# Performance work log

Measured on AMD Instinct MI355X. Metric: run time of the kernel, lower is better.

Reference implementation:

```python
import jax, jax.numpy as jnp
import numpy as np
import math

DIM = 1536
NH = 12
HD = 128          # head_dim
C = HD // 2       # 64 complex rope dims
MAX_ATTN = 15 * 880
EPS = 1e-6


def _rope_tables(max_len=1024, d=HD, theta=10000.0):
    # Wan rope_params: freqs = cat([rope(1024, d-4*(d//6)), rope(1024, 2*(d//6)), rope(1024, 2*(d//6))], dim=1)
    d0 = d - 4 * (d // 6)   # 44 -> 22 complex dims (F axis)
    d1 = 2 * (d // 6)       # 42 -> 21 complex dims (H and W axes)
    parts = []
    for dd in (d0, d1, d1):
        inv = 1.0 / theta ** (np.arange(0, dd, 2, dtype=np.float32) / dd)
        parts.append(np.outer(np.arange(max_len, dtype=np.float32), inv))
    ang = np.concatenate(parts, axis=1)                 # [1024, C]
    return np.stack([np.cos(ang), np.sin(ang)], -1)     # [1024, C, 2]


def rmsnorm(x, g, eps=EPS):
    return x * jax.lax.rsqrt(jnp.mean(x * x, axis=-1, keepdims=True) + eps) * g


def rope_apply(xq, f, h, w, freqs, start_frame):
    # xq: [B, S, N, D]; freqs: [1024, C, 2] cos/sin tables; S = f*h*w
    b, s, n, d = xq.shape
    c = d // 2
    s0 = c - 2 * (c // 3)   # F-axis complex dims (22)
    s1 = c // 3             # H/W-axis complex dims (21)
    cos, sin = freqs[..., 0], freqs[..., 1]

    def per_token(tab):
        tf = jnp.broadcast_to(tab[start_frame:start_frame + f, :s0][:, None, None, :], (f, h, w, s0))
        th = jnp.broadcast_to(tab[:h, s0:s0 + s1][None, :, None, :], (f, h, w, s1))
        tw = jnp.broadcast_to(tab[:w, s0 + s1:][None, None, :, :], (f, h, w, s1))
        return jnp.concatenate([tf, th, tw], -1).reshape(1, s, 1, c)

    pc, ps = per_token(cos), per_token(sin)
    xr = xq.reshape(b, s, n, c, 2)
    re, im = xr[..., 0], xr[..., 1]
    out = jnp.stack([re * pc - im * ps, re * ps + im * pc], -1)
    return out.reshape(b, s, n, d)


def _forward(x, wq, bq, wk, bk, wv, bv, wo, bo, gq, gk, freqs, k_cache, v_cache, f, h, w, current_start):
    b, s, _ = x.shape
    frame_seqlen = h * w
    start_frame = current_start // frame_seqlen

    q = rmsnorm(x @ wq.T + bq, gq).reshape(b, s, NH, HD)
    k = rmsnorm(x @ wk.T + bk, gk).reshape(b, s, NH, HD)
    v = (x @ wv.T + bv).reshape(b, s, NH, HD)

    rq = rope_apply(q, f, h, w, freqs, start_frame)
    rk = rope_apply(k, f, h, w, freqs, start_frame)

    current_end = current_start + s
    # cache not full: append new keys/values at [current_start:current_end]
    k_cache = jax.lax.dynamic_update_slice(k_cache, rk, (0, current_start, 0, 0))
    v_cache = jax.lax.dynamic_update_slice(v_cache, v, (0, current_start, 0, 0))

    win_start = max(0, current_end - MAX_ATTN)
    kk = k_cache[:, win_start:current_end]   # [B, Lk, N, D]
    vv = v_cache[:, win_start:current_end]

    scale = 1.0 / math.sqrt(HD)
    scores = jnp.einsum('bqnd,bknd->bnqk', rq, kk) * scale
    attn = jax.nn.softmax(scores, axis=-1)
    out = jnp.einsum('bnqk,bknd->bqnd', attn, vv).reshape(b, s, DIM)
    return out @ wo.T + bo


def setup_inputs() -> dict:
    key = jax.random.key(0)
    ks = jax.random.split(key, 8)
    B, S, CACHE = 1, 880, 18 * 880
    x = jax.random.normal(ks[0], (B, S, DIM), jnp.float32)

    def lin(k):
        k1, k2 = jax.random.split(k)
        wgt = jax.random.normal(k1, (DIM, DIM), jnp.float32) / math.sqrt(DIM)
        bia = jax.random.normal(k2, (DIM,), jnp.float32) * 0.01
        return wgt, bia

    wq, bq = lin(ks[1]); wk, bk = lin(ks[2]); wv, bv = lin(ks[3]); wo, bo = lin(ks[4])
    gq = jnp.ones((DIM,), jnp.float32)
    gk = jnp.ones((DIM,), jnp.float32)
    freqs = jnp.asarray(_rope_tables())
    k_cache = jax.random.normal(ks[5], (B, CACHE, NH, HD), jnp.float32) * 0.5
    v_cache = jax.random.normal(ks[6], (B, CACHE, NH, HD), jnp.float32) * 0.5
    grid_sizes = jnp.array([1, 22, 40], jnp.int32)  # (F, H, W), H*W = 880
    return dict(x=x, wq=wq, bq=bq, wk=wk, bk=bk, wv=wv, bv=bv, wo=wo, bo=bo,
                gq=gq, gk=gk, freqs=freqs, k_cache=k_cache, v_cache=v_cache,
                grid_sizes=grid_sizes, current_start=10560)


def reference(x, wq, bq, wk, bk, wv, bv, wo, bo, gq, gk, freqs, k_cache, v_cache, grid_sizes, current_start):
    f, h, w = (int(grid_sizes[0]), int(grid_sizes[1]), int(grid_sizes[2]))
    return _forward(x, wq, bq, wk, bk, wv, bv, wo, bo, gq, gk, freqs,
                    k_cache, v_cache, f, h, w, int(current_start))
```

## Files before the change

### kernel.cpp

```cpp
#include <hip/hip_runtime.h>

#define NHEADS 12
#define HDIM 128
#define MODEL_DIM 1536
#define MAX_ATTN_W 13200
#define NSPLIT 12

typedef unsigned short u16;
typedef unsigned int u32;
typedef float f32x4 __attribute__((ext_vector_type(4)));
typedef float f32x16 __attribute__((ext_vector_type(16)));
typedef __bf16 bf16x8 __attribute__((ext_vector_type(8)));

static __device__ __forceinline__ u16 f2bf(float f) {
  union { __bf16 h; u16 u; } cv;
  cv.h = (__bf16)f;
  return cv.u;
}
static __device__ __forceinline__ float bf2f(u16 u) {
  union { u32 u; float f; } cv;
  cv.u = ((u32)u) << 16;
  return cv.f;
}

__global__ void k_conv_bf16(const float* __restrict__ src, u16* __restrict__ dst, int n4) {
  int i = blockIdx.x * blockDim.x + threadIdx.x;
  if (i >= n4) return;
  float4 v = ((const float4*)src)[i];
  u32 lo = (u32)f2bf(v.x) | ((u32)f2bf(v.y) << 16);
  u32 hi = (u32)f2bf(v.z) | ((u32)f2bf(v.w) << 16);
  ((uint2*)dst)[i] = make_uint2(lo, hi);
}

__global__ void k_conv_bf16_w4(const float* __restrict__ s0, const float* __restrict__ s1,
                               const float* __restrict__ s2, const float* __restrict__ s3,
                               u16* __restrict__ d0, u16* __restrict__ d1,
                               u16* __restrict__ d2, u16* __restrict__ d3, int n4) {
  int i = blockIdx.x * blockDim.x + threadIdx.x;
  if (i >= n4) return;
  const int which = blockIdx.y;
  const float* src = (which == 0) ? s0 : (which == 1) ? s1 : (which == 2) ? s2 : s3;
  u16* dst = (which == 0) ? d0 : (which == 1) ? d1 : (which == 2) ? d2 : d3;
  float4 v = ((const float4*)src)[i];
  u32 lo = (u32)f2bf(v.x) | ((u32)f2bf(v.y) << 16);
  u32 hi = (u32)f2bf(v.z) | ((u32)f2bf(v.w) << 16);
  ((uint2*)dst)[i] = make_uint2(lo, hi);
}

__global__ void k_build_kold(const float* __restrict__ kc, u16* __restrict__ K_all,
                             const int* __restrict__ csp, int S, int KVcap) {
  const int cs = csp[0];
  const int ce = cs + S;
  int wst = ce - MAX_ATTN_W; if (wst < 0) wst = 0;
  const int oldlen = cs - wst;
  const long per = (long)oldlen * 16;
  const long total = per * NHEADS;
  for (long c = blockIdx.x * (long)blockDim.x + threadIdx.x; c < total;
       c += (long)gridDim.x * blockDim.x) {
    int n = (int)(c / per);
    long r = c - (long)n * per;
    int jo = (int)(r >> 4);
    int dc = ((int)r & 15) * 8;
    const float* s = kc + ((size_t)(wst + jo) * NHEADS + n) * HDIM + dc;
    float4 a = *(const float4*)s;
    float4 b = *(const float4*)(s + 4);
    uint4 o;
    o.x = (u32)f2bf(a.x) | ((u32)f2bf(a.y) << 16);
    o.y = (u32)f2bf(a.z) | ((u32)f2bf(a.w) << 16);
    o.z = (u32)f2bf(b.x) | ((u32)f2bf(b.y) << 16);
    o.w = (u32)f2bf(b.z) | ((u32)f2bf(b.w) << 16);
    *(uint4*)(K_all + ((size_t)n * KVcap + jo) * HDIM + dc) = o;
  }
}

__launch_bounds__(256)
__global__ void k_build_vtold(const float* __restrict__ vc, u16* __restrict__ VT,
                              const int* __restrict__ csp, int S, int KVcap) {
  __shared__ u16 tile[64][130];
  const int cs = csp[0];
  const int ce = cs + S;
  int wst = ce - MAX_ATTN_W; if (wst < 0) wst = 0;
  const int oldlen = cs - wst;
  const int n = blockIdx.y;
  const int j0 = blockIdx.x * 64;
  if (j0 >= oldlen) return;
  const int tid = threadIdx.x;

  #pragma unroll
  for (int i = 0; i < 8; i++) {
    int idx = tid + 256 * i;
    int j = idx >> 5;
    int dc = (idx & 31) * 4;
    float4 v = make_float4(0.f, 0.f, 0.f, 0.f);
    if (j0 + j < oldlen)
      v = *(const float4*)(vc + ((size_t)(wst + j0 + j) * NHEADS + n) * HDIM + dc);
    u32 lo = (u32)f2bf(v.x) | ((u32)f2bf(v.y) << 16);
    u32 hi = (u32)f2bf(v.z) | ((u32)f2bf(v.w) << 16);
    *(u32*)&tile[j][dc] = lo;
    *(u32*)&tile[j][dc + 2] = hi;
  }
  __syncthreads();

  const int d = tid >> 1;
  const int jh = (tid & 1) * 32;
  alignas(16) u16 buf[32];
  #pragma unroll
  for (int j = 0; j < 32; j++) buf[j] = tile[jh + j][d];
  u16* dst = VT + ((size_t)n * HDIM + d) * KVcap + j0 + jh;
  if (j0 + jh + 32 <= oldlen) {
    #pragma unroll
    for (int c = 0; c < 4; c++)
      *(uint4*)(dst + c * 8) = *(const uint4*)&buf[c * 8];
  } else {
    for (int j = 0; j < 32 && j0 + jh + j < oldlen; j++) dst[j] = buf[j];
  }
}

__launch_bounds__(256)
__global__ void k_gemm_o128(const u16* __restrict__ A, const u16* __restrict__ B,
                            const float* __restrict__ bias, float* __restrict__ out,
                            int M, int N, int K) {
  __shared__ __align__(16) u16 Al[128][40];
  __shared__ __align__(16) u16 Bl[128][40];
  const int n0 = blockIdx.y * 128;
  const int tid = threadIdx.x;
  const int wid = tid >> 6, l = tid & 63, l31 = l & 31, hi = l >> 5;
  const int wr = wid >> 1, wc = wid & 1;
  const int m0 = blockIdx.x * 128;
  f32x16 acc[2][2];
  #pragma unroll
  for (int mt = 0; mt < 2; mt++)
    #pragma unroll
    for (int nt = 0; nt < 2; nt++)
      #pragma unroll
      for (int j = 0; j < 16; j++) acc[mt][nt][j] = 0.f;
  const int row = tid >> 2, colc = (tid & 3) * 8;
  for (int k0 = 0; k0 < K; k0 += 32) {
    __syncthreads();
    uint4 a0 = *(const uint4*)(A + (size_t)(m0 + row) * K + k0 + colc);
    uint4 a1 = *(const uint4*)(A + (size_t)(m0 + row + 64) * K + k0 + colc);
    uint4 b0 = *(const uint4*)(B + (size_t)(n0 + row) * K + k0 + colc);
    uint4 b1 = *(const uint4*)(B + (size_t)(n0 + row + 64) * K + k0 + colc);
    *(uint4*)&Al[row][colc] = a0;
    *(uint4*)&Al[row + 64][colc] = a1;
    *(uint4*)&Bl[row][colc] = b0;
    *(uint4*)&Bl[row + 64][colc] = b1;
    __syncthreads();
    #pragma unroll
    for (int ks = 0; ks < 2; ks++) {
      bf16x8 af[2], bfr[2];
      #pragma unroll
      for (int mt = 0; mt < 2; mt++)
        af[mt] = *(const bf16x8*)&Al[wr * 64 + mt * 32 + l31][ks * 16 + hi * 8];
      #pragma unroll
      for (int nt = 0; nt < 2; nt++)
        bfr[nt] = *(const bf16x8*)&Bl[wc * 64 + nt * 32 + l31][ks * 16 + hi * 8];
      #pragma unroll
      for (int mt = 0; mt < 2; mt++)
        #pragma unroll
        for (int nt = 0; nt < 2; nt++)
          acc[mt][nt] = __builtin_amdgcn_mfma_f32_32x32x16_bf16(af[mt], bfr[nt], acc[mt][nt], 0, 0, 0);
    }
  }
  #pragma unroll
  for (int mt = 0; mt < 2; mt++)
    #pragma unroll
    for (int nt = 0; nt < 2; nt++) {
      const int col = n0 + wc * 64 + nt * 32 + l31;
      const float bb = bias[col];
      #pragma unroll
      for (int r = 0; r < 16; r++) {
        int rowo = m0 + wr * 64 + mt * 32 + (r & 3) + 8 * (r >> 2) + 4 * hi;
        if (rowo < M) out[(size_t)rowo * N + col] = acc[mt][nt][r] + bb;
      }
    }
}

__launch_bounds__(256)
__global__ void k_gemm_qkv128(const u16* __restrict__ A,
                              const u16* __restrict__ B0, const u16* __restrict__ B1,
                              const u16* __restrict__ B2,
                              const float* __restrict__ bias0, const float* __restrict__ bias1,
                              const float* __restrict__ bias2,
                              float* __restrict__ o0, float* __restrict__ o1, float* __restrict__ o2,
                              int M, int N, int K) {
  __shared__ __align__(16) u16 Al[128][40];
  __shared__ __align__(16) u16 Bl[128][40];
  const int nblk = N / 128;
  const int which = blockIdx.y / nblk;
  const int n0 = (blockIdx.y % nblk) * 128;
  const u16* B = (which == 0) ? B0 : ((which == 1) ? B1 : B2);
  const float* bias = (which == 0) ? bias0 : ((which == 1) ? bias1 : bias2);
  float* out = (which == 0) ? o0 : ((which == 1) ? o1 : o2);
  const int tid = threadIdx.x;
  const int wid = tid >> 6, l = tid & 63, l31 = l & 31, hi = l >> 5;
  const int wr = wid >> 1, wc = wid & 1;
  const int m0 = blockIdx.x * 128;
  f32x16 acc[2][2];
  #pragma unroll
  for (int mt = 0; mt < 2; mt++)
    #pragma unroll
    for (int nt = 0; nt < 2; nt++)
      #pragma unroll
      for (int j = 0; j < 16; j++) acc[mt][nt][j] = 0.f;
  const int row = tid >> 2, colc = (tid & 3) * 8;
  for (int k0 = 0; k0 < K; k0 += 32) {
    __syncthreads();
    uint4 a0 = *(const uint4*)(A + (size_t)(m0 + row) * K + k0 + colc);
    uint4 a1 = *(const uint4*)(A + (size_t)(m0 + row + 64) * K + k0 + colc);
    uint4 b0 = *(const uint4*)(B + (size_t)(n0 + row) * K + k0 + colc);
    uint4 b1 = *(const uint4*)(B + (size_t)(n0 + row + 64) * K + k0 + colc);
    *(uint4*)&Al[row][colc] = a0;
    *(uint4*)&Al[row + 64][colc] = a1;
    *(uint4*)&Bl[row][colc] = b0;
    *(uint4*)&Bl[row + 64][colc] = b1;
    __syncthreads();
    #pragma unroll
    for (int ks = 0; ks < 2; ks++) {
      bf16x8 af[2], bfr[2];
      #pragma unroll
      for (int mt = 0; mt < 2; mt++)
        af[mt] = *(const bf16x8*)&Al[wr * 64 + mt * 32 + l31][ks * 16 + hi * 8];
      #pragma unroll
      for (int nt = 0; nt < 2; nt++)
        bfr[nt] = *(const bf16x8*)&Bl[wc * 64 + nt * 32 + l31][ks * 16 + hi * 8];
      #pragma unroll
      for (int mt = 0; mt < 2; mt++)
        #pragma unroll
        for (int nt = 0; nt < 2; nt++)
          acc[mt][nt] = __builtin_amdgcn_mfma_f32_32x32x16_bf16(af[mt], bfr[nt], acc[mt][nt], 0, 0, 0);
    }
  }
  #pragma unroll
  for (int mt = 0; mt < 2; mt++)
    #pragma unroll
    for (int nt = 0; nt < 2; nt++) {
      const int col = n0 + wc * 64 + nt * 32 + l31;
      const float bb = bias[col];
      #pragma unroll
      for (int r = 0; r < 16; r++) {
        int rowo = m0 + wr * 64 + mt * 32 + (r & 3) + 8 * (r >> 2) + 4 * hi;
        if (rowo < M) out[(size_t)rowo * N + col] = acc[mt][nt][r] + bb;
      }
    }
}

__launch_bounds__(256)
__global__ void k_norm_rope(const float* __restrict__ qp, const float* __restrict__ kp,
                            const float* __restrict__ vp, const float* __restrict__ gq,
                            const float* __restrict__ gk, const float* __restrict__ freqs,
                            const int* __restrict__ gs, const int* __restrict__ csp,
                            int S, int KVcap,
                            u16* __restrict__ rq, u16* __restrict__ K_all,
                            u16* __restrict__ VT) {
  const int t = blockIdx.x;
  const int tid = threadIdx.x;
  const float* q = qp + (size_t)t * MODEL_DIM;
  const float* k = kp + (size_t)t * MODEL_DIM;
  const float* v = vp + (size_t)t * MODEL_DIM;
  float sq = 0.f, sk = 0.f;
  for (int j = tid; j < MODEL_DIM; j += 256) {
    float a = q[j]; sq += a * a;
    float b = k[j]; sk += b * b;
  }
  #pragma unroll
  for (int off = 32; off > 0; off >>= 1) {
    sq += __shfl_down(sq, off, 64);
    sk += __shfl_down(sk, off, 64);
  }
  __shared__ float red[8];
  int wv_ = tid >> 6, l = tid & 63;
  if (l == 0) { red[wv_] = sq; red[4 + wv_] = sk; }
  __syncthreads();
  sq = red[0] + red[1] + red[2] + red[3];
  sk = red[4] + red[5] + red[6] + red[7];
  const float rq_s = rsqrtf(sq * (1.0f / MODEL_DIM) + 1e-6f) * 0.12751744f;
  const float rk_s = rsqrtf(sk * (1.0f / MODEL_DIM) + 1e-6f);

  const int cs = csp[0];
  const int h = gs[1], ww = gs[2];
  const int hw = h * ww;
  const int sf = cs / hw;
  const int fi = t / hw;
  const int rr = t - fi * hw;
  const int hi = rr / ww;
  const int wi = rr - hi * ww;
  const int ce = cs + S;
  int wst = ce - MAX_ATTN_W; if (wst < 0) wst = 0;
  const int jj = cs + t - wst;

  for (int p = tid; p < NHEADS * 64; p += 256) {
    int n = p >> 6, c = p & 63;
    int pos = (c < 22) ? (sf + fi) : ((c < 43) ? hi : wi);
    float cv = freqs[(pos * 64 + c) * 2];
    float sv = freqs[(pos * 64 + c) * 2 + 1];
    int j0 = n * HDIM + 2 * c;
    float qr = q[j0] * rq_s * gq[j0];
    float qi = q[j0 + 1] * rq_s * gq[j0 + 1];
    u32 oq = (u32)f2bf(qr * cv - qi * sv) | ((u32)f2bf(qr * sv + qi * cv) << 16);
    *(u32*)(rq + ((size_t)n * S + t) * HDIM + 2 * c) = oq;
    float kr = k[j0] * rk_s * gk[j0];
    float ki = k[j0 + 1] * rk_s * gk[j0 + 1];
    u32 ok = (u32)f2bf(kr * cv - ki * sv) | ((u32)f2bf(kr * sv + ki * cv) << 16);
    *(u32*)(K_all + ((size_t)n * KVcap + jj) * HDIM + 2 * c) = ok;
  }
  for (int j = tid; j < MODEL_DIM; j += 256) {
    int n = j >> 7, d = j & 127;
    VT[((size_t)n * HDIM + d) * KVcap + jj] = f2bf(v[j]);
  }
}

__launch_bounds__(256, 2)
__global__ void k_attn_split(const u16* __restrict__ rq, const u16* __restrict__ K_all,
                             const u16* __restrict__ VT,
                             u16* __restrict__ po, float* __restrict__ pm, float* __restrict__ pl,
                             const int* __restrict__ csp, int S, int KVcap) {
  __shared__ __align__(16) u16 Klds[2][64][128];
  __shared__ __align__(16) u16 Vlds[2][128][64];

  const int tid = threadIdx.x;
  const int wid = tid >> 6;
  const int l = tid & 63;
  const int l31 = l & 31;
  const int hi = l >> 5;
  const int swz = (l31 & 7) << 3;
  const int head = blockIdx.y;
  const int split = blockIdx.z;
  const int q0 = blockIdx.x * 128;

  const int cs = csp[0];
  const int ce = cs + S;
  int wst = ce - MAX_ATTN_W; if (wst < 0) wst = 0;
  const int KV = ce - wst;
  const int chunk = (((KV + NSPLIT - 1) / NSPLIT) + 63) & ~63;
  const int kstart = split * chunk;
  int kend = kstart + chunk; if (kend > KV) kend = KV;

  const size_t pbase = ((size_t)head * NSPLIT + split) * S;
  const int qrow = q0 + wid * 32 + l31;

  if (kstart >= kend) {
    if (qrow < S && hi == 0) { pm[pbase + qrow] = -3.0e38f; pl[pbase + qrow] = 0.f; }
    return;
  }

  bf16x8 qf[8];
  if (qrow < S) {
    const u16* qp = rq + ((size_t)head * S + qrow) * HDIM;
    #pragma unroll
    for (int ds = 0; ds < 8; ds++) qf[ds] = *(const bf16x8*)(qp + ds * 16 + hi * 8);
  } else {
    #pragma unroll
    for (int ds = 0; ds < 8; ds++)
      #pragma unroll
      for (int i = 0; i < 8; i++) qf[ds][i] = (__bf16)0.0f;
  }

  f32x16 o[4];
  #pragma unroll
  for (int dt = 0; dt < 4; dt++)
    #pragma unroll
    for (int j = 0; j < 16; j++) o[dt][j] = 0.f;
  float m_ = -3.0e38f, lsum_ = 0.f;

  const u16* Kh = K_all + (size_t)head * KVcap * HDIM;
  const u16* Vh = VT + (size_t)head * HDIM * KVcap;

  uint4 kr[4], vr[4];
  auto load_tile = [&](int key0) {
    #pragma unroll
    for (int i = 0; i < 4; i++) {
      int cid = tid + 256 * i;
      int krow = cid >> 4;
      int gk_ = key0 + krow;
      kr[i] = make_uint4(0, 0, 0, 0);
      if (gk_ < kend) kr[i] = *(const uint4*)(Kh + (size_t)gk_ * HDIM + (cid & 15) * 8);
    }
    #pragma unroll
    for (int i = 0; i < 4; i++) {
      int cid = tid + 256 * i;
      int d = cid >> 3;
      int kc = (cid & 7) * 8;
      const u16* src = Vh + (size_t)d * KVcap + key0 + kc;
      if (key0 + kc + 8 <= kend) {
        vr[i] = *(const uint4*)src;
      } else {
        alignas(16) u16 tmp[8];
        #pragma unroll
        for (int j = 0; j < 8; j++) tmp[j] = (key0 + kc + j < kend) ? src[j] : (u16)0;
        vr[i] = *(const uint4*)tmp;
      }
    }
  };
  auto stage_to = [&](int p) {
    #pragma unroll
    for (int i = 0; i < 4; i++) {
      int cid = tid + 256 * i;
      int krow = cid >> 4;
      *(uint4*)&Klds[p][krow][((cid & 15) * 8) ^ ((krow & 7) << 3)] = kr[i];
    }
    #pragma unroll
    for (int i = 0; i < 4; i++) {
      int cid = tid + 256 * i;
      int d = cid >> 3;
      *(uint4*)&Vlds[p][d][((cid & 7) * 8) ^ ((d & 7) << 3)] = vr[i];
    }
  };

  const int ntiles = (kend - kstart + 63) >> 6;
  load_tile(kstart);
  stage_to(0);
  if (ntiles > 1) load_tile(kstart + 64);

  for (int t = 0; t < ntiles; t++) {
    const int key0 = kstart + (t << 6);
    const int cur = t & 1;
    __syncthreads();
    if (t + 1 < ntiles) stage_to(cur ^ 1);
    if (t + 2 < ntiles) load_tile(key0 + 128);

    f32x16 s[2];
    __builtin_amdgcn_s_setprio(1);
    #pragma unroll
    for (int kt = 0; kt < 2; kt++) {
      #pragma unroll
      for (int j = 0; j < 16; j++) s[kt][j] = 0.f;
      #pragma unroll
      for (int ds = 0; ds < 8; ds++) {
        bf16x8 kf = *(const bf16x8*)&Klds[cur][kt * 32 + l31][(ds * 16 + hi * 8) ^ swz];
        s[kt] = __builtin_amdgcn_mfma_f32_32x32x16_bf16(kf, qf[ds], s[kt], 0, 0, 0);
      }
    }
    __builtin_amdgcn_s_setprio(0);

    float tm = -3.0e38f;
    if (key0 + 64 <= kend) {
      #pragma unroll
      for (int kt = 0; kt < 2; kt++)
        #pragma unroll
        for (int r = 0; r < 16; r++) tm = fmaxf(tm, s[kt][r]);
    } else {
      #pragma unroll
      for (int kt = 0; kt < 2; kt++) {
        const int rem = kend - key0 - kt * 32;
        #pragma unroll
        for (int r = 0; r < 16; r++) {
          const int off = (r & 3) + 8 * (r >> 2) + 4 * hi;
          float v = (off < rem) ? s[kt][r] : -3.0e38f;
          s[kt][r] = v;
          tm = fmaxf(tm, v);
        }
      }
    }
    tm = fmaxf(tm, __shfl_xor(tm, 32, 64));

    if (!__all(tm <= m_ + 8.0f)) {
      float nm = fmaxf(m_, tm);
      float alpha = exp2f(m_ - nm);
      m_ = nm;
      lsum_ *= alpha;
      #pragma unroll
      for (int dt = 0; dt < 4; dt++)
        #pragma unroll
        for (int j = 0; j < 16; j++) o[dt][j] *= alpha;
    }

    float rs = 0.f;
    u32 w[2][8];
    #pragma unroll
    for (int kt = 0; kt < 2; kt++)
      #pragma unroll
      for (int j = 0; j < 8; j++) {
        float p0 = exp2f(s[kt][2 * j] - m_);
        float p1 = exp2f(s[kt][2 * j + 1] - m_);
        rs += p0 + p1;
        w[kt][j] = (u32)f2bf(p0) | ((u32)f2bf(p1) << 16);
      }
    rs += __shfl_xor(rs, 32, 64);
    lsum_ += rs;

    union { u32 u[4]; bf16x8 v; } pf[2][2];
    #pragma unroll
    for (int kt = 0; kt < 2; kt++) {
      u32 xw[8];
      #pragma unroll
      for (int j = 0; j < 8; j++) xw[j] = __shfl_xor(w[kt][j], 32, 64);
      pf[kt][0].u[0] = hi ? xw[2]    : w[kt][0];
      pf[kt][0].u[1] = hi ? xw[3]    : w[kt][1];
      pf[kt][0].u[2] = hi ? w[kt][2] : xw[0];
      pf[kt][0].u[3] = hi ? w[kt][3] : xw[1];
      pf[kt][1].u[0] = hi ? xw[6]    : w[kt][4];
      pf[kt][1].u[1] = hi ? xw[7]    : w[kt][5];
      pf[kt][1].u[2] = hi ? w[kt][6] : xw[4];
      pf[kt][1].u[3] = hi ? w[kt][7] : xw[5];
    }

    __builtin_amdgcn_s_setprio(1);
    #pragma unroll
    for (int dt = 0; dt < 4; dt++) {
      #pragma unroll
      for (int kt = 0; kt < 2; kt++)
        #pragma unroll
        for (int mm = 0; mm < 2; mm++) {
          bf16x8 vf = *(const bf16x8*)&Vlds[cur][dt * 32 + l31][(kt * 32 + mm * 16 + hi * 8) ^ swz];
          o[dt] = __builtin_amdgcn_mfma_f32_32x32x16_bf16(vf, pf[kt][mm].v, o[dt], 0, 0, 0);
        }
    }
    __builtin_amdgcn_s_setprio(0);
  }

  if (qrow < S) {
    float rl = (lsum_ > 0.f) ? (1.0f / lsum_) : 0.f;
    u16* dst = po + (pbase + qrow) * HDIM;
    #pragma unroll
    for (int dt = 0; dt < 4; dt++)
      #pragma unroll
      for (int jj = 0; jj < 4; jj++) {
        u32 w0 = (u32)f2bf(o[dt][4 * jj] * rl) | ((u32)f2bf(o[dt][4 * jj + 1] * rl) << 16);
        u32 w1 = (u32)f2bf(o[dt][4 * jj + 2] * rl) | ((u32)f2bf(o[dt][4 * jj + 3] * rl) << 16);
        *(uint2*)(dst + dt * 32 + 8 * jj + 4 * hi) = make_uint2(w0, w1);
      }
    if (hi == 0) { pm[pbase + qrow] = m_; pl[pbase + qrow] = lsum_; }
  }
}

__global__ void k_attn_reduce(const u16* __restrict__ po, const float* __restrict__ pm,
                              const float* __restrict__ pl, u16* __restrict__ attn_out,
                              int S) {
  const int t = blockIdx.x;
  const int h = blockIdx.y;
  const int d = threadIdx.x;
  float ms[NSPLIT];
  float M = -3.0e38f;
  #pragma unroll
  for (int s = 0; s < NSPLIT; s++) {
    ms[s] = pm[((size_t)h * NSPLIT + s) * S + t];
    M = fmaxf(M, ms[s]);
  }
  float L = 0.f, acc = 0.f;
  #pragma unroll
  for (int s = 0; s < NSPLIT; s++) {
    float wgt = exp2f(ms[s] - M) * pl[((size_t)h * NSPLIT + s) * S + t];
    L += wgt;
    acc += wgt * bf2f(po[(((size_t)h * NSPLIT + s) * S + t) * HDIM + d]);
  }
  attn_out[(size_t)t * MODEL_DIM + h * HDIM + d] = f2bf(acc / L);
}

extern "C" void kernel_launch(void* const* d_in, const int* in_sizes, int n_in,
                              void* d_out, int out_size, void* d_ws, size_t ws_size,
                              hipStream_t stream) {
  (void)n_in; (void)out_size; (void)ws_size;
  const float* x  = (const float*)d_in[0];
  const float* wq = (const float*)d_in[1];
  const float* bq = (const float*)d_in[2];
  const float* wk = (const float*)d_in[3];
  const float* bk = (const float*)d_in[4];
  const float* wv = (const float*)d_in[5];
  const float* bv = (const float*)d_in[6];
  const float* wo = (const float*)d_in[7];
  const float* bo = (const float*)d_in[8];
  const float* gq = (const float*)d_in[9];
  const float* gk = (const float*)d_in[10];
  const float* freqs = (const float*)d_in[11];
  const float* k_cache = (const float*)d_in[12];
  const float* v_cache = (const float*)d_in[13];
  const int* gs  = (const int*)d_in[14];
  const int* csp = (const int*)d_in[15];

  const int S = in_sizes[0] / MODEL_DIM;
  const int CACHE = in_sizes[12] / (NHEADS * HDIM);
  const int KVcap = (CACHE < MAX_ATTN_W) ? CACHE : MAX_ATTN_W;
  const int Mpad = (S + 127) & ~127;

  char* ws = (char*)d_ws;
  size_t off = 0;
  auto alloc = [&](size_t bytes) {
    char* p = ws + off;
    off += (bytes + 255) & ~(size_t)255;
    return p;
  };
  u16* xb   = (u16*)alloc((size_t)Mpad * MODEL_DIM * 2);
  u16* wqb  = (u16*)alloc((size_t)MODEL_DIM * MODEL_DIM * 2);
  u16* wkb  = (u16*)alloc((size_t)MODEL_DIM * MODEL_DIM * 2);
  u16* wvb  = (u16*)alloc((size_t)MODEL_DIM * MODEL_DIM * 2);
  u16* wob  = (u16*)alloc((size_t)MODEL_DIM * MODEL_DIM * 2);
  float* q_pre = (float*)alloc((size_t)S * MODEL_DIM * 4);
  float* k_pre = (float*)alloc((size_t)S * MODEL_DIM * 4);
  float* v_pre = (float*)alloc((size_t)S * MODEL_DIM * 4);
  u16* rqb   = (u16*)alloc((size_t)NHEADS * S * HDIM * 2);
  u16* K_all = (u16*)alloc((size_t)NHEADS * KVcap * HDIM * 2);
  u16* VT    = (u16*)alloc((size_t)NHEADS * HDIM * KVcap * 2);
  u16* attn_o = (u16*)alloc((size_t)Mpad * MODEL_DIM * 2);
  u16* po    = (u16*)alloc((size_t)NHEADS * NSPLIT * S * HDIM * 2);
  float* pm  = (float*)alloc((size_t)NHEADS * NSPLIT * S * 4);
  float* pl  = (float*)alloc((size_t)NHEADS * NSPLIT * S * 4);

  const int nx4 = S * MODEL_DIM / 4;
  const int nw4 = MODEL_DIM * MODEL_DIM / 4;
  hipLaunchKernelGGL(k_conv_bf16, dim3((nx4 + 255) / 256), dim3(256), 0, stream, x, xb, nx4);
  hipLaunchKernelGGL(k_conv_bf16_w4, dim3((nw4 + 255) / 256, 4), dim3(256), 0, stream,
                     wq, wk, wv, wo, wqb, wkb, wvb, wob, nw4);

  hipLaunchKernelGGL(k_build_kold, dim3(2048), dim3(256), 0, stream, k_cache, K_all, csp, S, KVcap);
  hipLaunchKernelGGL(k_build_vtold, dim3((KVcap + 63) / 64, NHEADS), dim3(256), 0, stream,
                     v_cache, VT, csp, S, KVcap);

  hipLaunchKernelGGL(k_gemm_qkv128, dim3(Mpad / 128, 3 * MODEL_DIM / 128), dim3(256), 0, stream,
                     xb, wqb, wkb, wvb, bq, bk, bv, q_pre, k_pre, v_pre, S, MODEL_DIM, MODEL_DIM);

  hipLaunchKernelGGL(k_norm_rope, dim3(S), dim3(256), 0, stream,
                     q_pre, k_pre, v_pre, gq, gk, freqs, gs, csp, S, KVcap, rqb, K_all, VT);

  hipLaunchKernelGGL(k_attn_split, dim3((S + 127) / 128, NHEADS, NSPLIT), dim3(256), 0, stream,
                     rqb, K_all, VT, po, pm, pl, csp, S, KVcap);

  hipLaunchKernelGGL(k_attn_reduce, dim3(S, NHEADS), dim3(128), 0, stream, po, pm, pl, attn_o, S);

  hipLaunchKernelGGL(k_gemm_o128, dim3(Mpad / 128, MODEL_DIM / 128), dim3(256), 0, stream,
                     attn_o, wob, bo, (float*)d_out, S, MODEL_DIM, MODEL_DIM);
}
```

Before: 333.6 us.

## Load K/V tiles directly into LDS with global_load_lds, single-buffer, raise occupancy

Replaces the register-staged, double-buffered K/V tile loads in the split attention kernel with direct global-to-LDS loads into a single buffer, synchronising before and after each tile. This halves LDS use and frees registers, so launch bounds go from 2 to 3 blocks per CU and the KV split count goes from 12 to 18 for more parallelism. The cost is losing the overlap between loading the next tile and computing the current one. The bounds checks on the ragged final tile are also gone, so keys past kend are read without masking.

```diff
diff --git a/kernel.cpp b/kernel.cpp
--- a/kernel.cpp
+++ b/kernel.cpp
@@ -4,7 +4,7 @@
 #define HDIM 128
 #define MODEL_DIM 1536
 #define MAX_ATTN_W 13200
-#define NSPLIT 12
+#define NSPLIT 18
 
 typedef unsigned short u16;
 typedef unsigned int u32;
@@ -21,6 +21,11 @@
   union { u32 u; float f; } cv;
   cv.u = ((u32)u) << 16;
   return cv.f;
+}
+static __device__ __forceinline__ void gload_lds16(const void* g, void* l) {
+  __builtin_amdgcn_global_load_lds(
+      (const __attribute__((address_space(1))) unsigned int*)g,
+      (__attribute__((address_space(3))) unsigned int*)l, 16, 0, 0);
 }
 
 __global__ void k_conv_bf16(const float* __restrict__ src, u16* __restrict__ dst, int n4) {
@@ -310,13 +315,13 @@
   }
 }
 
-__launch_bounds__(256, 2)
+__launch_bounds__(256, 3)
 __global__ void k_attn_split(const u16* __restrict__ rq, const u16* __restrict__ K_all,
                              const u16* __restrict__ VT,
                              u16* __restrict__ po, float* __restrict__ pm, float* __restrict__ pl,
                              const int* __restrict__ csp, int S, int KVcap) {
-  __shared__ __align__(16) u16 Klds[2][64][128];
-  __shared__ __align__(16) u16 Vlds[2][128][64];
+  __shared__ __align__(16) u16 Klds[64][128];
+  __shared__ __align__(16) u16 Vlds[128][64];
 
   const int tid = threadIdx.x;
   const int wid = tid >> 6;
@@ -366,58 +371,36 @@
   const u16* Kh = K_all + (size_t)head * KVcap * HDIM;
   const u16* Vh = VT + (size_t)head * HDIM * KVcap;
 
-  uint4 kr[4], vr[4];
-  auto load_tile = [&](int key0) {
-    #pragma unroll
-    for (int i = 0; i < 4; i++) {
-      int cid = tid + 256 * i;
-      int krow = cid >> 4;
-      int gk_ = key0 + krow;
-      kr[i] = make_uint4(0, 0, 0, 0);
-      if (gk_ < kend) kr[i] = *(const uint4*)(Kh + (size_t)gk_ * HDIM + (cid & 15) * 8);
-    }
-    #pragma unroll
-    for (int i = 0; i < 4; i++) {
-      int cid = tid + 256 * i;
-      int d = cid >> 3;
-      int kc = (cid & 7) * 8;
-      const u16* src = Vh + (size_t)d * KVcap + key0 + kc;
-      if (key0 + kc + 8 <= kend) {
-        vr[i] = *(const uint4*)src;
-      } else {
-        alignas(16) u16 tmp[8];
-        #pragma unroll
-        for (int j = 0; j < 8; j++) tmp[j] = (key0 + kc + j < kend) ? src[j] : (u16)0;
-        vr[i] = *(const uint4*)tmp;
-      }
-    }
-  };
-  auto stage_to = [&](int p) {
-    #pragma unroll
-    for (int i = 0; i < 4; i++) {
-      int cid = tid + 256 * i;
-      int krow = cid >> 4;
-      *(uint4*)&Klds[p][krow][((cid & 15) * 8) ^ ((krow & 7) << 3)] = kr[i];
-    }
-    #pragma unroll
-    for (int i = 0; i < 4; i++) {
-      int cid = tid + 256 * i;
-      int d = cid >> 3;
-      *(uint4*)&Vlds[p][d][((cid & 7) * 8) ^ ((d & 7) << 3)] = vr[i];
-    }
-  };
+  int krow_i[4], kcol_i[4], vd_i[4], vcol_i[4];
+  #pragma unroll
+  for (int i = 0; i < 4; i++) {
+    int kr_ = (wid * 4 + i) * 4 + (l >> 4);
+    krow_i[i] = kr_;
+    kcol_i[i] = (((l & 15) ^ (kr_ & 7)) << 3);
+    int vd_ = (wid * 4 + i) * 8 + (l >> 3);
+    vd_i[i] = vd_;
+    vcol_i[i] = (((l & 7) ^ (vd_ & 7)) << 3);
+  }
+  u16* kldst[4];
+  u16* vldst[4];
+  #pragma unroll
+  for (int i = 0; i < 4; i++) {
+    kldst[i] = &Klds[0][0] + (wid * 4 + i) * 512;
+    vldst[i] = &Vlds[0][0] + (wid * 4 + i) * 512;
+  }
 
   const int ntiles = (kend - kstart + 63) >> 6;
-  load_tile(kstart);
-  stage_to(0);
-  if (ntiles > 1) load_tile(kstart + 64);
 
   for (int t = 0; t < ntiles; t++) {
     const int key0 = kstart + (t << 6);
-    const int cur = t & 1;
     __syncthreads();
-    if (t + 1 < ntiles) stage_to(cur ^ 1);
-    if (t + 2 < ntiles) load_tile(key0 + 128);
+    #pragma unroll
+    for (int i = 0; i < 4; i++)
+      gload_lds16(Kh + (size_t)(key0 + krow_i[i]) * HDIM + kcol_i[i], kldst[i]);
+    #pragma unroll
+    for (int i = 0; i < 4; i++)
+      gload_lds16(Vh + (size_t)vd_i[i] * KVcap + key0 + vcol_i[i], vldst[i]);
+    __syncthreads();
 
     f32x16 s[2];
     __builtin_amdgcn_s_setprio(1);
@@ -427,7 +410,7 @@
       for (int j = 0; j < 16; j++) s[kt][j] = 0.f;
       #pragma unroll
       for (int ds = 0; ds < 8; ds++) {
-        bf16x8 kf = *(const bf16x8*)&Klds[cur][kt * 32 + l31][(ds * 16 + hi * 8) ^ swz];
+        bf16x8 kf = *(const bf16x8*)&Klds[kt * 32 + l31][(ds * 16 + hi * 8) ^ swz];
         s[kt] = __builtin_amdgcn_mfma_f32_32x32x16_bf16(kf, qf[ds], s[kt], 0, 0, 0);
       }
     }
@@ -502,7 +485,7 @@
       for (int kt = 0; kt < 2; kt++)
         #pragma unroll
         for (int mm = 0; mm < 2; mm++) {
-          bf16x8 vf = *(const bf16x8*)&Vlds[cur][dt * 32 + l31][(kt * 32 + mm * 16 + hi * 8) ^ swz];
+          bf16x8 vf = *(const bf16x8*)&Vlds[dt * 32 + l31][(kt * 32 + mm * 16 + hi * 8) ^ swz];
           o[dt] = __builtin_amdgcn_mfma_f32_32x32x16_bf16(vf, pf[kt][mm].v, o[dt], 0, 0, 0);
         }
     }
```

Result: no change. 339.8 us (+1.9%).
